# Optimization experiments

Measured on AMD Instinct MI355X. Metric: run time of the kernel, lower is better.

Reference implementation:

```python
import jax, jax.numpy as jnp
import numpy as np

EPS_IN = 1e-5  # torch InstanceNorm1d default eps


def instance_norm(x):
    # x: [B, C, L]; normalize over L per (B, C); no affine (torch default)
    m = jnp.mean(x, axis=-1, keepdims=True)
    v = jnp.var(x, axis=-1, keepdims=True)
    return (x - m) / jnp.sqrt(v + EPS_IN)


def conv1x1(x, w, b):
    # x: [B, Cin, L], w: [Cout, Cin], b: [Cout]
    return jnp.einsum('bcl,oc->bol', x, w) + b[None, :, None]


def _window_indices(L_dec, L_enc, window, stride):
    # static (numpy) window layout matching the torch while-loop
    starts = list(range(0, L_dec, stride))
    dec_ends = [min(s + window, L_dec) for s in starts]
    enc_se = [(int(s * L_enc / L_dec), min(int(e * L_enc / L_dec), L_enc))
              for s, e in zip(starts, dec_ends)]
    max_enc = max(ee - es for es, ee in enc_se)
    ar_d = np.arange(window)
    ar_e = np.arange(max_enc)
    dec_idx = np.stack([np.clip(s + ar_d, 0, L_dec - 1) for s in starts])          # [NW, Wd]
    dec_valid = np.stack([(s + ar_d) < e for s, e in zip(starts, dec_ends)])       # [NW, Wd]
    enc_idx = np.stack([np.clip(es + ar_e, 0, L_enc - 1) for es, ee in enc_se])    # [NW, We]
    enc_valid = np.stack([(es + ar_e) < ee for es, ee in enc_se])                  # [NW, We]
    return (jnp.asarray(dec_idx), jnp.asarray(dec_valid),
            jnp.asarray(enc_idx), jnp.asarray(enc_valid))


def setup_inputs() -> dict:
    key = jax.random.key(0)
    ks = jax.random.split(key, 16)
    B, Cd, Ce, Ld, Le = 4, 512, 256, 4096, 8192
    H = 4 * Cd  # mlp hidden
    s = 0.02
    return {
        'x_decoder': jax.random.normal(ks[0], (B, Cd, Ld), jnp.float32),
        'x_encoder': jax.random.normal(ks[1], (B, Ce, Le), jnp.float32),
        'wq': jax.random.normal(ks[2], (Cd, Cd), jnp.float32) * s,
        'bq': jnp.zeros((Cd,), jnp.float32),
        'wk': jax.random.normal(ks[3], (Cd, Ce), jnp.float32) * s,
        'bk': jnp.zeros((Cd,), jnp.float32),
        'wv': jax.random.normal(ks[4], (Cd, Ce), jnp.float32) * s,
        'bv': jnp.zeros((Cd,), jnp.float32),
        'wo': jax.random.normal(ks[5], (Cd, Cd), jnp.float32) * s,
        'bo': jnp.zeros((Cd,), jnp.float32),
        'w1': jax.random.normal(ks[6], (H, Cd), jnp.float32) * s,
        'b1': jnp.zeros((H,), jnp.float32),
        'w2': jax.random.normal(ks[7], (Cd, H), jnp.float32) * s,
        'b2': jnp.zeros((Cd,), jnp.float32),
    }


NUM_HEADS = 8
WINDOW = 256
STRIDE = 192  # int(256 * (1 - 0.25))


def reference(x_decoder, x_encoder, wq, bq, wk, bk, wv, bv, wo, bo, w1, b1, w2, b2):
    B, Cd, Ld = x_decoder.shape
    Le = x_encoder.shape[-1]
    nh, hd = NUM_HEADS, Cd // NUM_HEADS
    residual = x_decoder

    q = instance_norm(conv1x1(x_decoder, wq, bq))
    k = instance_norm(conv1x1(x_encoder, wk, bk))
    v = instance_norm(conv1x1(x_encoder, wv, bv))

    # [B, C, L] -> [B, nh, L, hd]
    q = q.reshape(B, nh, hd, Ld).transpose(0, 1, 3, 2)
    k = k.reshape(B, nh, hd, Le).transpose(0, 1, 3, 2)
    v = v.reshape(B, nh, hd, Le).transpose(0, 1, 3, 2)

    dec_idx, dec_valid, enc_idx, enc_valid = _window_indices(Ld, Le, WINDOW, STRIDE)
    # gather all windows at once
    qw = q[:, :, dec_idx, :]  # [B, nh, NW, Wd, hd]
    kw = k[:, :, enc_idx, :]  # [B, nh, NW, We, hd]
    vw = v[:, :, enc_idx, :]

    scale = hd ** -0.5
    scores = jnp.einsum('bhnqd,bhnkd->bhnqk', qw, kw) * scale
    scores = jnp.where(enc_valid[None, None, :, None, :], scores, jnp.float32(-1e30))
    attn = jax.nn.softmax(scores, axis=-1)
    win = jnp.einsum('bhnqk,bhnkd->bhnqd', attn, vw)
    win = win * dec_valid[None, None, :, :, None].astype(win.dtype)

    # scatter-add overlapping windows then average by overlap count
    flat_idx = dec_idx.reshape(-1)  # [NW*Wd]
    out = jnp.zeros((B, nh, Ld, hd), win.dtype).at[:, :, flat_idx, :].add(
        win.reshape(B, nh, -1, hd))
    counts = jnp.zeros((Ld,), win.dtype).at[flat_idx].add(
        dec_valid.reshape(-1).astype(win.dtype))
    out = out / jnp.clip(counts, 1e-8)[None, None, :, None]

    attn_out = out.transpose(0, 1, 3, 2).reshape(B, Cd, Ld)
    x = instance_norm(conv1x1(attn_out, wo, bo)) + residual

    # AttentionMLP1D (dropout inactive in eval)
    h = jax.nn.gelu(conv1x1(x, w1, b1), approximate=False)
    y = instance_norm(conv1x1(h, w2, b2))
    return y + x
```

## Files before the change

kernel.cpp:

```cpp
#include <hip/hip_runtime.h>
#include <hip/hip_bf16.h>
#include <math.h>
#include <stdint.h>

#define LDD 4096
#define LEE 8192
#define CDIM 512
#define CENC 256
#define HDIM 2048
#define NB 4
#define NHEAD 8
#define HD 64
#define NWIN 22
#define WINQ 256
#define WSTRIDE 192
#define KVS 1024

typedef __attribute__((ext_vector_type(8))) short bf16x8;
typedef __attribute__((ext_vector_type(8))) unsigned short u16x8;
typedef __attribute__((ext_vector_type(4))) float f32x4;
typedef __attribute__((ext_vector_type(16))) float f32x16;
typedef __attribute__((ext_vector_type(2))) unsigned int u32x2;
typedef __attribute__((ext_vector_type(4))) unsigned int u32x4;
typedef unsigned short ushort_t;

__device__ __forceinline__ uint32_t pack2(float lo, float hi) {
    return ((__float_as_uint(hi) + 0x8000u) & 0xffff0000u) |
           ((__float_as_uint(lo) + 0x8000u) >> 16);
}
__device__ __forceinline__ ushort_t bfc(float x) {
    return (ushort_t)((__float_as_uint(x) + 0x8000u) >> 16);
}
__device__ __forceinline__ float bf2f(ushort_t u) {
    return __uint_as_float(((uint32_t)u) << 16);
}
__device__ __forceinline__ void gload16(const void* g, void* l) {
    __builtin_amdgcn_global_load_lds(
        (const __attribute__((address_space(1))) void*)g,
        (__attribute__((address_space(3))) void*)l, 16, 0, 0);
}
__device__ __forceinline__ float gelu_fast(float x) {
    float z = fabsf(x) * 0.70710678f;
    float t = 1.0f / fmaf(0.3275911f, z, 1.0f);
    float p = t * fmaf(t, fmaf(t, fmaf(t, fmaf(t, 1.061405429f, -1.453152027f),
                                        1.421413741f), -0.284496736f), 0.254829592f);
    float e = __expf(-z * z);
    float erfz = fmaf(-p, e, 1.0f);
    float sgn = copysignf(erfz, x);
    return 0.5f * x * (1.0f + sgn);
}

struct Cvt6Args {
    const float* src[6];
    ushort_t* dst[6];
    int n[6];
};
__global__ __launch_bounds__(256)
void cvt6(Cvt6Args a)
{
    int seg = blockIdx.y;
    int i = (blockIdx.x * 256 + threadIdx.x) * 4;
    if (i < a.n[seg]) {
        float4 v = *reinterpret_cast<const float4*>(&a.src[seg][i]);
        u32x2 p; p[0] = pack2(v.x, v.y); p[1] = pack2(v.z, v.w);
        *reinterpret_cast<u32x2*>(&a.dst[seg][i]) = p;
    }
}

__global__ __launch_bounds__(256)
void bias_stack(const float* __restrict__ bk, const float* __restrict__ bv,
                float* __restrict__ bkv)
{
    int t = blockIdx.x * 256 + threadIdx.x;
    bkv[t] = (t < 512) ? bk[t] : bv[t - 512];
}

__global__ __launch_bounds__(256)
void tcvt(const float* __restrict__ in, ushort_t* __restrict__ outb, int C, int L)
{
    __shared__ float T[64][65];
    int l0 = blockIdx.x * 64, c0 = blockIdx.y * 64, b = blockIdx.z;
    int tid = threadIdx.x;
    int ll = tid & 63, cq = tid >> 6;
    #pragma unroll
    for (int i = 0; i < 16; ++i) {
        int c = cq + i * 4;
        T[c][ll] = in[((size_t)b * C + c0 + c) * L + l0 + ll];
    }
    __syncthreads();
    int cc = tid & 63, lq = tid >> 6;
    #pragma unroll
    for (int i = 0; i < 16; ++i) {
        int l = lq + i * 4;
        outb[((size_t)b * L + l0 + l) * C + c0 + cc] = bfc(T[cc][l]);
    }
}

template<int EPI, int STATS>
__global__ __launch_bounds__(256)
void mgemm2(const ushort_t* __restrict__ A, const ushort_t* __restrict__ Wt,
            const float* __restrict__ bias, ushort_t* __restrict__ Out,
            float* __restrict__ part, int M, int N, int K)
{
    __shared__ __align__(16) ushort_t As[2][8192];
    __shared__ __align__(16) ushort_t Bs[2][8192];

    int Nt = gridDim.x;
    int flat = blockIdx.y * Nt + blockIdx.x;
    int nwg = Nt * gridDim.y;
    int swz = (flat & 7) * (nwg >> 3) + (flat >> 3);
    int nb = swz % Nt, mb = swz / Nt;
    int b = blockIdx.z;
    int m0 = mb * 128, n0 = nb * 128;

    int tid = threadIdx.x;
    int lane = tid & 63;
    int w = tid >> 6;
    int q16 = lane & 15, g = lane >> 4;
    int wr = w >> 1, wc = w & 1;

    const ushort_t* Ag[4]; const ushort_t* Wg[4];
    #pragma unroll
    for (int i = 0; i < 4; ++i) {
        int gran = w * 256 + i * 64 + lane;
        int row = gran >> 3;
        int c8 = (gran & 7) ^ (row & 7);
        Ag[i] = A + ((size_t)b * M + m0 + row) * K + c8 * 8;
        Wg[i] = Wt + ((size_t)(n0 + row)) * K + c8 * 8;
    }

    f32x4 acc[4][4];
    #pragma unroll
    for (int mt = 0; mt < 4; ++mt)
        #pragma unroll
        for (int nt = 0; nt < 4; ++nt) {
            acc[mt][nt][0] = 0.f; acc[mt][nt][1] = 0.f;
            acc[mt][nt][2] = 0.f; acc[mt][nt][3] = 0.f;
        }

    #pragma unroll
    for (int i = 0; i < 4; ++i) {
        gload16(Ag[i], &As[0][w * 2048 + i * 512]);
        gload16(Wg[i], &Bs[0][w * 2048 + i * 512]);
    }

    int NTILES = K >> 6;
    for (int kt = 0; kt < NTILES; ++kt) {
        int cur = kt & 1;
        __syncthreads();
        if (kt + 1 < NTILES) {
            int k0 = (kt + 1) << 6;
            #pragma unroll
            for (int i = 0; i < 4; ++i) {
                gload16(Ag[i] + k0, &As[cur ^ 1][w * 2048 + i * 512]);
                gload16(Wg[i] + k0, &Bs[cur ^ 1][w * 2048 + i * 512]);
            }
        }
        const char* Ab = (const char*)&As[cur][0];
        const char* Bb = (const char*)&Bs[cur][0];
        bf16x8 ka[4][2], kb[4][2];
        #pragma unroll
        for (int mt = 0; mt < 4; ++mt) {
            int r = wr * 64 + mt * 16 + q16;
            int rb = r * 128;
            int sw8 = (r & 7) << 4;
            ka[mt][0] = *reinterpret_cast<const bf16x8*>(Ab + rb + ((g * 16) ^ sw8));
            ka[mt][1] = *reinterpret_cast<const bf16x8*>(Ab + rb + ((64 + g * 16) ^ sw8));
        }
        #pragma unroll
        for (int nt = 0; nt < 4; ++nt) {
            int r = wc * 64 + nt * 16 + q16;
            int rb = r * 128;
            int sw8 = (r & 7) << 4;
            kb[nt][0] = *reinterpret_cast<const bf16x8*>(Bb + rb + ((g * 16) ^ sw8));
            kb[nt][1] = *reinterpret_cast<const bf16x8*>(Bb + rb + ((64 + g * 16) ^ sw8));
        }
        #pragma unroll
        for (int mt = 0; mt < 4; ++mt)
            #pragma unroll
            for (int nt = 0; nt < 4; ++nt) {
                acc[mt][nt] = __builtin_amdgcn_mfma_f32_16x16x32_bf16(kb[nt][0], ka[mt][0], acc[mt][nt], 0, 0, 0);
                acc[mt][nt] = __builtin_amdgcn_mfma_f32_16x16x32_bf16(kb[nt][1], ka[mt][1], acc[mt][nt], 0, 0, 0);
            }
    }

    float4 bv4[4];
    #pragma unroll
    for (int nt = 0; nt < 4; ++nt)
        bv4[nt] = *reinterpret_cast<const float4*>(&bias[n0 + wc * 64 + nt * 16 + g * 4]);

    float s_[4][4], q_[4][4];
    if (STATS) {
        #pragma unroll
        for (int nt = 0; nt < 4; ++nt)
            #pragma unroll
            for (int r = 0; r < 4; ++r) { s_[nt][r] = 0.f; q_[nt][r] = 0.f; }
    }

    #pragma unroll
    for (int mt = 0; mt < 4; ++mt) {
        int m = m0 + wr * 64 + mt * 16 + q16;
        size_t rowoff = ((size_t)b * M + m) * N;
        #pragma unroll
        for (int nt = 0; nt < 4; ++nt) {
            float vv[4];
            #pragma unroll
            for (int r = 0; r < 4; ++r) {
                float val = acc[mt][nt][r] + ((const float*)&bv4[nt])[r];
                if (EPI == 1) val = gelu_fast(val);
                if (STATS) { s_[nt][r] += val; q_[nt][r] = fmaf(val, val, q_[nt][r]); }
                vv[r] = val;
            }
            u32x2 pk; pk[0] = pack2(vv[0], vv[1]); pk[1] = pack2(vv[2], vv[3]);
            *reinterpret_cast<u32x2*>(&Out[rowoff + n0 + wc * 64 + nt * 16 + g * 4]) = pk;
        }
    }

    if (STATS) {
        __syncthreads();
        float* SS = (float*)&As[0][0];
        float* SQ = (float*)&Bs[0][0];
        #pragma unroll
        for (int nt = 0; nt < 4; ++nt)
            #pragma unroll
            for (int r = 0; r < 4; ++r) {
                int nl = wc * 64 + nt * 16 + g * 4 + r;
                SS[nl * 33 + wr * 16 + q16] = s_[nt][r];
                SQ[nl * 33 + wr * 16 + q16] = q_[nt][r];
            }
        __syncthreads();
        if (tid < 128) {
            float ts = 0.f, tq = 0.f;
            #pragma unroll 8
            for (int j = 0; j < 32; ++j) { ts += SS[tid * 33 + j]; tq += SQ[tid * 33 + j]; }
            size_t po = (((size_t)b * (M >> 7) + mb) * N + n0 + tid) * 2;
            part[po] = ts; part[po + 1] = tq;
        }
    }
}

__global__ __launch_bounds__(256)
void stats_finish(const float* __restrict__ pq, const float* __restrict__ pkv,
                  float* __restrict__ qm, float* __restrict__ qr,
                  float* __restrict__ vm, float* __restrict__ vr, float qscale)
{
    int id = blockIdx.x * 256 + threadIdx.x;
    int b = id >> 9, c = id & 511;
    float sq = 0.f, qq = 0.f;
    for (int sp = 0; sp < 32; ++sp) {
        size_t po = (((size_t)(b * 32 + sp)) * CDIM + c) * 2;
        sq += pq[po]; qq += pq[po + 1];
    }
    float sk = 0.f, qk = 0.f, sv = 0.f, qv = 0.f;
    for (int sp = 0; sp < 64; ++sp) {
        size_t po = (((size_t)(b * 64 + sp)) * KVS + c) * 2;
        sk += pkv[po]; qk += pkv[po + 1];
        sv += pkv[po + 1024]; qv += pkv[po + 1025];
    }
    float mq = sq / (float)LDD;
    float rq = rsqrtf(qq / (float)LDD - mq * mq + 1e-5f);
    float mk = sk / (float)LEE;
    float rk = rsqrtf(qk / (float)LEE - mk * mk + 1e-5f);
    float mv = sv / (float)LEE;
    qm[id] = mq;
    qr[id] = rq * rk * qscale;
    vm[id] = mv;
    vr[id] = rsqrtf(qv / (float)LEE - mv * mv + 1e-5f);
}

template<int RES>
__global__ __launch_bounds__(256)
void cn_apply_v(const ushort_t* __restrict__ in, const float* __restrict__ part,
                const ushort_t* __restrict__ res, ushort_t* __restrict__ out,
                int L, int SPLITM)
{
    __shared__ float SM[CDIM], SR[CDIM];
    int b = blockIdx.z;
    int tid = threadIdx.x;
    for (int c = tid; c < CDIM; c += 256) {
        float fs = 0.f, fq = 0.f;
        for (int sp = 0; sp < SPLITM; ++sp) {
            size_t po = (((size_t)b * SPLITM + sp) * CDIM + c) * 2;
            fs += part[po]; fq += part[po + 1];
        }
        float mean = fs / (float)L;
        float var = fq / (float)L - mean * mean;
        SM[c] = mean; SR[c] = rsqrtf(var + 1e-5f);
    }
    __syncthreads();
    int c0 = (tid & 63) * 8;
    int l0 = blockIdx.x * 16 + (tid >> 6) * 4;
    float mm[8], rr[8];
    #pragma unroll
    for (int j = 0; j < 8; ++j) { mm[j] = SM[c0 + j]; rr[j] = SR[c0 + j]; }
    #pragma unroll
    for (int i = 0; i < 4; ++i) {
        int l = l0 + i;
        size_t off = ((size_t)b * L + l) * CDIM + c0;
        u16x8 v = *reinterpret_cast<const u16x8*>(in + off);
        u16x8 rv;
        if (RES) rv = *reinterpret_cast<const u16x8*>(res + off);
        u16x8 o;
        #pragma unroll
        for (int j = 0; j < 8; ++j) {
            float y = (bf2f((ushort_t)v[j]) - mm[j]) * rr[j];
            if (RES) y += bf2f((ushort_t)rv[j]);
            o[j] = bfc(y);
        }
        *reinterpret_cast<u16x8*>(out + off) = o;
    }
}

__global__ __launch_bounds__(256)
void cn_apply_t(const ushort_t* __restrict__ in, const float* __restrict__ part,
                const ushort_t* __restrict__ res, float* __restrict__ outf,
                int L, int SPLITM)
{
    __shared__ float SM[64], SR[64];
    __shared__ float T[64][65];
    int b = blockIdx.z;
    int c0 = blockIdx.x * 64;
    int l0 = blockIdx.y * 64;
    int tid = threadIdx.x;
    if (tid < 64) {
        int c = c0 + tid;
        float fs = 0.f, fq = 0.f;
        for (int sp = 0; sp < SPLITM; ++sp) {
            size_t po = (((size_t)b * SPLITM + sp) * CDIM + c) * 2;
            fs += part[po]; fq += part[po + 1];
        }
        float mean = fs / (float)L;
        float var = fq / (float)L - mean * mean;
        SM[tid] = mean; SR[tid] = rsqrtf(var + 1e-5f);
    }
    __syncthreads();
    int cc = tid & 63;
    int lq = tid >> 6;
    float mean = SM[cc], rstd = SR[cc];
    #pragma unroll
    for (int i = 0; i < 16; ++i) {
        int l = l0 + lq + i * 4;
        size_t idx = ((size_t)b * L + l) * CDIM + c0 + cc;
        T[lq + i * 4][cc] = (bf2f(in[idx]) - mean) * rstd + bf2f(res[idx]);
    }
    __syncthreads();
    int ll = tid & 63;
    int cr = tid >> 6;
    #pragma unroll
    for (int i = 0; i < 16; ++i) {
        int c = cr + i * 4;
        outf[((size_t)b * CDIM + c0 + c) * L + l0 + ll] = T[ll][c];
    }
}

__global__ __launch_bounds__(512, 2)
void attn_win_mfma32(const ushort_t* __restrict__ qT, const ushort_t* __restrict__ kvT,
                     const float* __restrict__ qmean, const float* __restrict__ qrs,
                     const float* __restrict__ vmean, const float* __restrict__ vrstd,
                     ushort_t* __restrict__ win)
{
    __shared__ __align__(16) char KB[3][8192];
    __shared__ __align__(16) ushort_t VBv[2][64][68];
    __shared__ float VMS[64], VRS[64], QMS[64], QRS[64];

    int p = blockIdx.x;
    int xcd = p & 7;
    int sub = p >> 3;
    int g9 = xcd * 11 + (sub % 11);
    int hh = sub / 11;
    int n = g9 % 22, b = g9 / 22;

    int s = n * WSTRIDE;
    int es = 2 * s;
    bool tail = (n == NWIN - 1);
    int nch = tail ? 2 : 8;

    int tid = threadIdx.x;
    int lane = tid & 63;
    int w = tid >> 6;
    int l31 = lane & 31;
    int hf = lane >> 5;
    bool active = (!tail) || (w < 2);

    const ushort_t* kbase = kvT + ((size_t)b * LEE + es) * KVS + hh * HD;
    const ushort_t* vbase = kbase + 512;

    int vc8 = tid & 7;
    int vkp = tid >> 3;
    bool vdo = (tid < 256);
    int vcs = (vc8 & 6) << 2;

    int kpos0 = tid >> 3;
    int kc8 = (tid & 7) ^ (kpos0 & 7);
    const ushort_t* ksrc = kbase + (size_t)kpos0 * KVS + kc8 * 8;

    u16x8 qraw[4];
    if (active) {
        int qrow_g = s + w * 32 + l31;
        const ushort_t* qp = qT + ((size_t)b * LDD + qrow_g) * CDIM + hh * HD;
        #pragma unroll
        for (int kd = 0; kd < 4; ++kd)
            qraw[kd] = *reinterpret_cast<const u16x8*>(qp + kd * 16 + hf * 8);
    }
    gload16(ksrc, &KB[0][tid * 16]);
    u16x8 wa0, wb0;
    if (vdo) {
        const ushort_t* src = vbase + (size_t)(2 * vkp) * KVS + vc8 * 8;
        wa0 = *reinterpret_cast<const u16x8*>(src);
        wb0 = *reinterpret_cast<const u16x8*>(src + KVS);
    }
    gload16(ksrc + (size_t)64 * KVS, &KB[1][tid * 16]);
    if (tid < 64) {
        int c = b * CDIM + hh * HD + tid;
        VMS[tid] = vmean[c]; VRS[tid] = vrstd[c];
        QMS[tid] = qmean[c]; QRS[tid] = qrs[c];
    }
    if (vdo) {
        #pragma unroll
        for (int j = 0; j < 8; ++j) {
            int d = vc8 * 8 + j;
            uint32_t dw = (uint32_t)wa0[j] | ((uint32_t)wb0[j] << 16);
            *reinterpret_cast<uint32_t*>(&VBv[0][d][(2 * vkp) ^ vcs]) = dw;
        }
    }
    asm volatile("s_waitcnt lgkmcnt(0)" ::: "memory");
    __builtin_amdgcn_s_barrier();

    bf16x8 bq[4];
    if (active) {
        #pragma unroll
        for (int kd = 0; kd < 4; ++kd) {
            u32x4 pk;
            #pragma unroll
            for (int jj = 0; jj < 4; ++jj) {
                int c0 = kd * 16 + hf * 8 + 2 * jj;
                float y0 = (bf2f((ushort_t)qraw[kd][2 * jj]) - QMS[c0]) * QRS[c0];
                float y1 = (bf2f((ushort_t)qraw[kd][2 * jj + 1]) - QMS[c0 + 1]) * QRS[c0 + 1];
                pk[jj] = pack2(y0, y1);
            }
            bq[kd] = __builtin_bit_cast(bf16x8, pk);
        }
    }

    f32x16 acc0, acc1;
    #pragma unroll
    for (int e = 0; e < 16; ++e) { acc0[e] = 0.f; acc1[e] = 0.f; }
    float ssum = 0.f;
    int swk = (lane & 7) << 4;
    int vrs0 = ((l31 >> 3) & 6) << 2;
    int vrs1 = (((l31 + 32) >> 3) & 6) << 2;

    for (int ch = 0; ch < nch; ++ch) {
        asm volatile("s_waitcnt vmcnt(1) lgkmcnt(0)" ::: "memory");
        __builtin_amdgcn_s_barrier();

        u16x8 wa, wb;
        bool pfv = (ch + 1 < nch);
        if (pfv && vdo) {
            const ushort_t* src = vbase + (size_t)((ch + 1) * 64 + 2 * vkp) * KVS + vc8 * 8;
            wa = *reinterpret_cast<const u16x8*>(src);
            wb = *reinterpret_cast<const u16x8*>(src + KVS);
        }
        if (ch + 2 < nch)
            gload16(ksrc + (size_t)((ch + 2) * 64) * KVS, &KB[(ch + 2) % 3][tid * 16]);

        if (active) {
            f32x16 st0, st1;
            #pragma unroll
            for (int e = 0; e < 16; ++e) { st0[e] = 0.f; st1[e] = 0.f; }
            const char* KA0 = &KB[ch % 3][l31 * 128];
            const char* KA1 = KA0 + 32 * 128;
            __builtin_amdgcn_s_setprio(1);
            #pragma unroll
            for (int kd = 0; kd < 4; ++kd) {
                int co = (kd * 32 + hf * 16) ^ swk;
                bf16x8 ka0 = *reinterpret_cast<const bf16x8*>(KA0 + co);
                bf16x8 ka1 = *reinterpret_cast<const bf16x8*>(KA1 + co);
                st0 = __builtin_amdgcn_mfma_f32_32x32x16_bf16(ka0, bq[kd], st0, 0, 0, 0);
                st1 = __builtin_amdgcn_mfma_f32_32x32x16_bf16(ka1, bq[kd], st1, 0, 0, 0);
            }
            __builtin_amdgcn_s_setprio(0);
            uint32_t pk0[8], pk1[8];
            float ls = 0.f;
            #pragma unroll
            for (int pp = 0; pp < 8; ++pp) {
                float a = exp2f(st0[2 * pp] - 24.f), bb = exp2f(st0[2 * pp + 1] - 24.f);
                float c = exp2f(st1[2 * pp] - 24.f), dd = exp2f(st1[2 * pp + 1] - 24.f);
                ls += (a + bb) + (c + dd);
                pk0[pp] = pack2(a, bb);
                pk1[pp] = pack2(c, dd);
            }
            ssum += ls;
            __builtin_amdgcn_s_setprio(1);
            #pragma unroll
            for (int kc = 0; kc < 4; ++kc) {
                const int sub2 = kc & 1;
                uint32_t pA0, pA1, pA2, pA3;
                if ((kc >> 1) == 0) { pA0 = pk0[4*sub2]; pA1 = pk0[4*sub2+1]; pA2 = pk0[4*sub2+2]; pA3 = pk0[4*sub2+3]; }
                else                { pA0 = pk1[4*sub2]; pA1 = pk1[4*sub2+1]; pA2 = pk1[4*sub2+2]; pA3 = pk1[4*sub2+3]; }
                uint32_t s0 = hf ? pA0 : pA2;
                uint32_t s1 = hf ? pA1 : pA3;
                uint32_t r0 = (uint32_t)__shfl_xor((int)s0, 32);
                uint32_t r1 = (uint32_t)__shfl_xor((int)s1, 32);
                u32x4 bt;
                bt[0] = hf ? r0 : pA0;
                bt[1] = hf ? r1 : pA1;
                bt[2] = hf ? pA2 : r0;
                bt[3] = hf ? pA3 : r1;
                bf16x8 pbf = __builtin_bit_cast(bf16x8, bt);
                int ko = kc * 16 + hf * 8;
                const uint32_t* vr0p = reinterpret_cast<const uint32_t*>(&VBv[ch & 1][l31][ko ^ vrs0]);
                const uint32_t* vr1p = reinterpret_cast<const uint32_t*>(&VBv[ch & 1][l31 + 32][ko ^ vrs1]);
                u32x2 alo = *reinterpret_cast<const u32x2*>(vr0p);
                u32x2 ahi = *reinterpret_cast<const u32x2*>(vr0p + 2);
                u32x2 blo = *reinterpret_cast<const u32x2*>(vr1p);
                u32x2 bhi = *reinterpret_cast<const u32x2*>(vr1p + 2);
                u32x4 va0u, va1u;
                va0u[0] = alo[0]; va0u[1] = alo[1]; va0u[2] = ahi[0]; va0u[3] = ahi[1];
                va1u[0] = blo[0]; va1u[1] = blo[1]; va1u[2] = bhi[0]; va1u[3] = bhi[1];
                bf16x8 va0 = __builtin_bit_cast(bf16x8, va0u);
                bf16x8 va1 = __builtin_bit_cast(bf16x8, va1u);
                acc0 = __builtin_amdgcn_mfma_f32_32x32x16_bf16(va0, pbf, acc0, 0, 0, 0);
                acc1 = __builtin_amdgcn_mfma_f32_32x32x16_bf16(va1, pbf, acc1, 0, 0, 0);
            }
            __builtin_amdgcn_s_setprio(0);
        }

        if (pfv && vdo) {
            #pragma unroll
            for (int j = 0; j < 8; ++j) {
                int d = vc8 * 8 + j;
                uint32_t dw = (uint32_t)wa[j] | ((uint32_t)wb[j] << 16);
                *reinterpret_cast<uint32_t*>(&VBv[(ch + 1) & 1][d][(2 * vkp) ^ vcs]) = dw;
            }
        }
    }

    if (active) {
        float stot = ssum + __shfl_xor(ssum, 32);
        float rs = 1.f / stot;
        size_t wbase = (((size_t)(b * NHEAD + hh) * NWIN + n) * WINQ + (size_t)(w * 32 + l31)) * HD;
        #pragma unroll
        for (int p4 = 0; p4 < 4; ++p4) {
            int d0 = p4 * 8 + hf * 4;
            float o0[4], o1[4];
            #pragma unroll
            for (int e = 0; e < 4; ++e) {
                o0[e] = VRS[d0 + e] * (acc0[4 * p4 + e] * rs - VMS[d0 + e]);
                o1[e] = VRS[32 + d0 + e] * (acc1[4 * p4 + e] * rs - VMS[32 + d0 + e]);
            }
            u32x2 w0, w1v;
            w0[0] = pack2(o0[0], o0[1]); w0[1] = pack2(o0[2], o0[3]);
            w1v[0] = pack2(o1[0], o1[1]); w1v[1] = pack2(o1[2], o1[3]);
            *reinterpret_cast<u32x2*>(&win[wbase + p4 * 8 + hf * 4]) = w0;
            *reinterpret_cast<u32x2*>(&win[wbase + 32 + p4 * 8 + hf * 4]) = w1v;
        }
    }
}

__global__ __launch_bounds__(256)
void attn_finalize(const ushort_t* __restrict__ win, ushort_t* __restrict__ outT)
{
    int l0 = blockIdx.x * 64;
    int hh = blockIdx.y, b = blockIdx.z;
    int tid = threadIdx.x;
    int d2 = tid & 31;
    int lq = tid >> 5;
    #pragma unroll
    for (int i = 0; i < 8; ++i) {
        int ll = lq + i * 8;
        int l = l0 + ll;
        int n1 = min(NWIN - 1, l / WSTRIDE);
        int n0 = (l >= 64) ? ((l - 64) / WSTRIDE) : 0;
        float a0 = 0.f, a1 = 0.f;
        for (int nn = n0; nn <= n1; ++nn) {
            int qrow = l - nn * WSTRIDE;
            uint32_t v = *reinterpret_cast<const uint32_t*>(
                &win[(((size_t)(b * NHEAD + hh) * NWIN + nn) * WINQ + qrow) * HD + d2 * 2]);
            a0 += bf2f((ushort_t)(v & 0xffffu));
            a1 += bf2f((ushort_t)(v >> 16));
        }
        float inv = 1.f / (float)(n1 - n0 + 1);
        uint32_t o = pack2(a0 * inv, a1 * inv);
        *reinterpret_cast<uint32_t*>(
            &outT[((size_t)b * LDD + l) * CDIM + hh * HD + d2 * 2]) = o;
    }
}

extern "C" void kernel_launch(void* const* d_in, const int* in_sizes, int n_in,
                              void* d_out, int out_size, void* d_ws, size_t ws_size,
                              hipStream_t stream)
{
    const float* x_dec = (const float*)d_in[0];
    const float* x_enc = (const float*)d_in[1];
    const float* wq = (const float*)d_in[2];
    const float* bq = (const float*)d_in[3];
    const float* wk = (const float*)d_in[4];
    const float* bk = (const float*)d_in[5];
    const float* wv = (const float*)d_in[6];
    const float* bv = (const float*)d_in[7];
    const float* wo = (const float*)d_in[8];
    const float* bo = (const float*)d_in[9];
    const float* w1 = (const float*)d_in[10];
    const float* b1 = (const float*)d_in[11];
    const float* w2 = (const float*)d_in[12];
    const float* b2 = (const float*)d_in[13];
    float* out = (float*)d_out;

    char* base = (char*)d_ws;
    ushort_t* wqb  = (ushort_t*)(base);
    ushort_t* wkvb = (ushort_t*)(base + 524288);
    ushort_t* wob  = (ushort_t*)(base + 1048576);
    ushort_t* w1b  = (ushort_t*)(base + 1572864);
    ushort_t* w2b  = (ushort_t*)(base + 3670016);
    ushort_t* x_decT_b = (ushort_t*)(base + 5767168);
    ushort_t* q_pre    = (ushort_t*)(base + 22544384);
    ushort_t* kvT      = (ushort_t*)(base + 39321600);
    ushort_t* x_encT_b = (ushort_t*)(base + 106430464);
    ushort_t* winb     = (ushort_t*)(base + 123207680);
    float*    partQ    = (float*)(base + 169345024);
    float*    partKV   = (float*)(base + 170393600);
    float*    qm       = (float*)(base + 172490752);
    float*    qr       = qm + 2048;
    float*    vm       = qr + 2048;
    float*    vrs      = vm + 2048;
    float*    bkv      = vrs + 2048;
    ushort_t* attn_outT = x_encT_b;
    ushort_t* xo_pre   = q_pre;
    ushort_t* hT       = kvT;
    ushort_t* y_pre    = winb;

    dim3 blk(256);
    dim3 blk512(512);

    Cvt6Args ca;
    ca.src[0] = wq; ca.src[1] = wk; ca.src[2] = wv;
    ca.src[3] = wo; ca.src[4] = w1; ca.src[5] = w2;
    ca.dst[0] = wqb; ca.dst[1] = wkvb; ca.dst[2] = wkvb + 131072;
    ca.dst[3] = wob; ca.dst[4] = w1b; ca.dst[5] = w2b;
    ca.n[0] = 262144; ca.n[1] = 131072; ca.n[2] = 131072;
    ca.n[3] = 262144; ca.n[4] = 1048576; ca.n[5] = 1048576;
    cvt6<<<dim3(1024, 6), blk, 0, stream>>>(ca);
    bias_stack<<<dim3(4), blk, 0, stream>>>(bk, bv, bkv);

    tcvt<<<dim3(LDD / 64, CDIM / 64, NB), blk, 0, stream>>>(x_dec, x_decT_b, CDIM, LDD);
    tcvt<<<dim3(LEE / 64, CENC / 64, NB), blk, 0, stream>>>(x_enc, x_encT_b, CENC, LEE);

    const float QSCALE = 0.125f * 1.4426950408889634f;

    mgemm2<0,1><<<dim3(CDIM / 128, LDD / 128, NB), blk, 0, stream>>>(x_decT_b, wqb, bq, q_pre, partQ, LDD, CDIM, CDIM);
    mgemm2<0,1><<<dim3(KVS / 128, LEE / 128, NB), blk, 0, stream>>>(x_encT_b, wkvb, bkv, kvT, partKV, LEE, KVS, CENC);
    stats_finish<<<dim3(8), blk, 0, stream>>>(partQ, partKV, qm, qr, vm, vrs, QSCALE);

    attn_win_mfma32<<<dim3(NWIN * NHEAD * NB), blk512, 0, stream>>>(q_pre, kvT, qm, qr, vm, vrs, winb);
    attn_finalize<<<dim3(LDD / 64, NHEAD, NB), blk, 0, stream>>>(winb, attn_outT);

    mgemm2<0,1><<<dim3(CDIM / 128, LDD / 128, NB), blk, 0, stream>>>(attn_outT, wob, bo, xo_pre, partQ, LDD, CDIM, CDIM);
    cn_apply_v<1><<<dim3(LDD / 16, 1, NB), blk, 0, stream>>>(xo_pre, partQ, x_decT_b, xo_pre, LDD, LDD / 128);

    mgemm2<1,0><<<dim3(HDIM / 128, LDD / 128, NB), blk, 0, stream>>>(xo_pre, w1b, b1, hT, nullptr, LDD, HDIM, CDIM);

    mgemm2<0,1><<<dim3(CDIM / 128, LDD / 128, NB), blk, 0, stream>>>(hT, w2b, b2, y_pre, partQ, LDD, CDIM, HDIM);
    cn_apply_t<<<dim3(CDIM / 64, LDD / 64, NB), blk, 0, stream>>>(y_pre, partQ, xo_pre, out, LDD, LDD / 128);

    (void)in_sizes; (void)n_in; (void)out_size; (void)ws_size;
}
```

Before: 331.8 us.

## Replace 128x128 GEMM with 256x256 eight-wave ping-pong pipelined kernel

Replaces the 128x128, 4-wave double-buffered bf16 MFMA GEMM with a 256x256 tile, 8-wave kernel. It splits each K-step into quarter tiles, staged through four LDS slots with explicit vmcnt/lgkmcnt waits, barriers and s_setprio around the MFMA bursts. The aim is more data reuse per LDS load and better overlap of global loads with matrix math. Statistic partials and stats_finish are re-parameterised for the new row-block count. The risk is that the larger tiles cut the grid to 128 blocks for the N=512 GEMMs, which may leave many CUs idle.

```diff
diff --git a/kernel.cpp b/kernel.cpp
--- a/kernel.cpp
+++ b/kernel.cpp
@@ -97,13 +97,13 @@
 }
 
 template<int EPI, int STATS>
-__global__ __launch_bounds__(256)
-void mgemm2(const ushort_t* __restrict__ A, const ushort_t* __restrict__ Wt,
-            const float* __restrict__ bias, ushort_t* __restrict__ Out,
-            float* __restrict__ part, int M, int N, int K)
-{
-    __shared__ __align__(16) ushort_t As[2][8192];
-    __shared__ __align__(16) ushort_t Bs[2][8192];
+__global__ __launch_bounds__(512, 1)
+void mgemm8p(const ushort_t* __restrict__ A, const ushort_t* __restrict__ Wt,
+             const float* __restrict__ bias, ushort_t* __restrict__ Out,
+             float* __restrict__ part, int M, int N, int K)
+{
+    __shared__ __align__(16) ushort_t Asl[4][8192];
+    __shared__ __align__(16) ushort_t Bsl[4][8192];
 
     int Nt = gridDim.x;
     int flat = blockIdx.y * Nt + blockIdx.x;
@@ -111,83 +111,205 @@
     int swz = (flat & 7) * (nwg >> 3) + (flat >> 3);
     int nb = swz % Nt, mb = swz / Nt;
     int b = blockIdx.z;
-    int m0 = mb * 128, n0 = nb * 128;
+    int m0 = mb * 256, n0 = nb * 256;
 
     int tid = threadIdx.x;
     int lane = tid & 63;
     int w = tid >> 6;
-    int q16 = lane & 15, g = lane >> 4;
-    int wr = w >> 1, wc = w & 1;
-
-    const ushort_t* Ag[4]; const ushort_t* Wg[4];
-    #pragma unroll
-    for (int i = 0; i < 4; ++i) {
-        int gran = w * 256 + i * 64 + lane;
-        int row = gran >> 3;
-        int c8 = (gran & 7) ^ (row & 7);
-        Ag[i] = A + ((size_t)b * M + m0 + row) * K + c8 * 8;
-        Wg[i] = Wt + ((size_t)(n0 + row)) * K + c8 * 8;
-    }
-
-    f32x4 acc[4][4];
-    #pragma unroll
-    for (int mt = 0; mt < 4; ++mt)
+    int q16 = lane & 15, g4 = lane >> 4;
+    int wr = w >> 2, wc = w & 3;
+
+    const ushort_t* Ap[2][2]; const ushort_t* Bp[2][2];
+    #pragma unroll
+    for (int j = 0; j < 2; ++j) {
+        int g = w * 128 + j * 64 + lane;
+        int row = g >> 3;
+        int c8 = (g & 7) ^ (row & 7);
+        #pragma unroll
+        for (int hh = 0; hh < 2; ++hh) {
+            Ap[hh][j] = A + ((size_t)b * M + m0 + hh * 128 + row) * K + c8 * 8;
+            Bp[hh][j] = Wt + ((size_t)(n0 + hh * 128 + row)) * K + c8 * 8;
+        }
+    }
+    int dbase = w * 2048;
+
+    auto stageA = [&](int slot, int hh, int k0) {
+        char* d = (char*)&Asl[0][0] + slot * 16384 + dbase;
+        gload16(Ap[hh][0] + k0, d);
+        gload16(Ap[hh][1] + k0, d + 1024);
+    };
+    auto stageB = [&](int slot, int hh, int k0) {
+        char* d = (char*)&Bsl[0][0] + slot * 16384 + dbase;
+        gload16(Bp[hh][0] + k0, d);
+        gload16(Bp[hh][1] + k0, d + 1024);
+    };
+
+    f32x4 acc[8][4];
+    #pragma unroll
+    for (int mt = 0; mt < 8; ++mt)
         #pragma unroll
         for (int nt = 0; nt < 4; ++nt) {
             acc[mt][nt][0] = 0.f; acc[mt][nt][1] = 0.f;
             acc[mt][nt][2] = 0.f; acc[mt][nt][3] = 0.f;
         }
 
-    #pragma unroll
-    for (int i = 0; i < 4; ++i) {
-        gload16(Ag[i], &As[0][w * 2048 + i * 512]);
-        gload16(Wg[i], &Bs[0][w * 2048 + i * 512]);
-    }
-
-    int NTILES = K >> 6;
-    for (int kt = 0; kt < NTILES; ++kt) {
-        int cur = kt & 1;
-        __syncthreads();
-        if (kt + 1 < NTILES) {
-            int k0 = (kt + 1) << 6;
-            #pragma unroll
-            for (int i = 0; i < 4; ++i) {
-                gload16(Ag[i] + k0, &As[cur ^ 1][w * 2048 + i * 512]);
-                gload16(Wg[i] + k0, &Bs[cur ^ 1][w * 2048 + i * 512]);
-            }
-        }
-        const char* Ab = (const char*)&As[cur][0];
-        const char* Bb = (const char*)&Bs[cur][0];
+    const char* As0 = (const char*)&Asl[wr][0];
+    const char* As1 = (const char*)&Asl[2 + wr][0];
+    const char* Bs0 = (const char*)&Bsl[wc >> 1][0];
+    const char* Bs1 = (const char*)&Bsl[2 + (wc >> 1)][0];
+
+    auto ldka = [&](const char* sp, int rbase, bf16x8 (&ka)[4][2]) {
+        #pragma unroll
+        for (int mt = 0; mt < 4; ++mt) {
+            int r = rbase + mt * 16 + q16;
+            int rb = r * 128, sw8 = (r & 7) << 4;
+            ka[mt][0] = *reinterpret_cast<const bf16x8*>(sp + rb + ((g4 * 16) ^ sw8));
+            ka[mt][1] = *reinterpret_cast<const bf16x8*>(sp + rb + ((64 + g4 * 16) ^ sw8));
+        }
+    };
+    auto ldkb = [&](const char* sp, bf16x8 (&kb)[4][2]) {
+        #pragma unroll
+        for (int nt = 0; nt < 4; ++nt) {
+            int r = (wc & 1) * 64 + nt * 16 + q16;
+            int rb = r * 128, sw8 = (r & 7) << 4;
+            kb[nt][0] = *reinterpret_cast<const bf16x8*>(sp + rb + ((g4 * 16) ^ sw8));
+            kb[nt][1] = *reinterpret_cast<const bf16x8*>(sp + rb + ((64 + g4 * 16) ^ sw8));
+        }
+    };
+
+    int NT = K >> 6;
+    int NI = NT >> 1;
+
+    stageB(0, 0, 0);
+    stageB(1, 1, 0);
+    stageA(0, 0, 0);
+    stageA(1, 1, 0);
+    stageB(2, 0, 64);
+    stageB(3, 1, 64);
+    stageA(2, 0, 64);
+
+    for (int i = 0; i < NI; ++i) {
         bf16x8 ka[4][2], kb[4][2];
-        #pragma unroll
-        for (int mt = 0; mt < 4; ++mt) {
-            int r = wr * 64 + mt * 16 + q16;
-            int rb = r * 128;
-            int sw8 = (r & 7) << 4;
-            ka[mt][0] = *reinterpret_cast<const bf16x8*>(Ab + rb + ((g * 16) ^ sw8));
-            ka[mt][1] = *reinterpret_cast<const bf16x8*>(Ab + rb + ((64 + g * 16) ^ sw8));
-        }
-        #pragma unroll
-        for (int nt = 0; nt < 4; ++nt) {
-            int r = wc * 64 + nt * 16 + q16;
-            int rb = r * 128;
-            int sw8 = (r & 7) << 4;
-            kb[nt][0] = *reinterpret_cast<const bf16x8*>(Bb + rb + ((g * 16) ^ sw8));
-            kb[nt][1] = *reinterpret_cast<const bf16x8*>(Bb + rb + ((64 + g * 16) ^ sw8));
-        }
+        int kB1 = (2 * i + 1) * 64;
+        int kA  = (2 * i + 2) * 64;
+        int kC  = (2 * i + 3) * 64;
+        bool pf = (i + 1 < NI);
+
+        asm volatile("s_waitcnt vmcnt(6) lgkmcnt(0)" ::: "memory");
+        __builtin_amdgcn_s_barrier();
+        asm volatile("" ::: "memory");
+        stageA(3, 1, kB1);
+        ldka(As0, 0, ka); ldkb(Bs0, kb);
+        __builtin_amdgcn_s_setprio(1);
         #pragma unroll
         for (int mt = 0; mt < 4; ++mt)
             #pragma unroll
-            for (int nt = 0; nt < 4; ++nt) {
+            for (int nt = 0; nt < 2; ++nt) {
                 acc[mt][nt] = __builtin_amdgcn_mfma_f32_16x16x32_bf16(kb[nt][0], ka[mt][0], acc[mt][nt], 0, 0, 0);
                 acc[mt][nt] = __builtin_amdgcn_mfma_f32_16x16x32_bf16(kb[nt][1], ka[mt][1], acc[mt][nt], 0, 0, 0);
             }
+        __builtin_amdgcn_s_setprio(0);
+        asm volatile("s_waitcnt lgkmcnt(0)" ::: "memory");
+        __builtin_amdgcn_s_barrier();
+        asm volatile("" ::: "memory");
+        if (pf) stageB(0, 0, kA);
+        __builtin_amdgcn_s_setprio(1);
+        #pragma unroll
+        for (int mt = 0; mt < 4; ++mt)
+            #pragma unroll
+            for (int nt = 2; nt < 4; ++nt) {
+                acc[mt][nt] = __builtin_amdgcn_mfma_f32_16x16x32_bf16(kb[nt][0], ka[mt][0], acc[mt][nt], 0, 0, 0);
+                acc[mt][nt] = __builtin_amdgcn_mfma_f32_16x16x32_bf16(kb[nt][1], ka[mt][1], acc[mt][nt], 0, 0, 0);
+            }
+        __builtin_amdgcn_s_setprio(0);
+        asm volatile("s_waitcnt lgkmcnt(0)" ::: "memory");
+        __builtin_amdgcn_s_barrier();
+        asm volatile("" ::: "memory");
+        if (pf) stageB(1, 1, kA);
+        ldka(As0, 64, ka);
+        __builtin_amdgcn_s_setprio(1);
+        #pragma unroll
+        for (int mt = 0; mt < 4; ++mt)
+            #pragma unroll
+            for (int nt = 0; nt < 2; ++nt) {
+                acc[4 + mt][nt] = __builtin_amdgcn_mfma_f32_16x16x32_bf16(kb[nt][0], ka[mt][0], acc[4 + mt][nt], 0, 0, 0);
+                acc[4 + mt][nt] = __builtin_amdgcn_mfma_f32_16x16x32_bf16(kb[nt][1], ka[mt][1], acc[4 + mt][nt], 0, 0, 0);
+            }
+        __builtin_amdgcn_s_setprio(0);
+        asm volatile("s_waitcnt lgkmcnt(0)" ::: "memory");
+        __builtin_amdgcn_s_barrier();
+        asm volatile("" ::: "memory");
+        if (pf) stageA(0, 0, kA);
+        __builtin_amdgcn_s_setprio(1);
+        #pragma unroll
+        for (int mt = 0; mt < 4; ++mt)
+            #pragma unroll
+            for (int nt = 2; nt < 4; ++nt) {
+                acc[4 + mt][nt] = __builtin_amdgcn_mfma_f32_16x16x32_bf16(kb[nt][0], ka[mt][0], acc[4 + mt][nt], 0, 0, 0);
+                acc[4 + mt][nt] = __builtin_amdgcn_mfma_f32_16x16x32_bf16(kb[nt][1], ka[mt][1], acc[4 + mt][nt], 0, 0, 0);
+            }
+        __builtin_amdgcn_s_setprio(0);
+        if (pf) asm volatile("s_waitcnt vmcnt(6) lgkmcnt(0)" ::: "memory");
+        else    asm volatile("s_waitcnt vmcnt(0) lgkmcnt(0)" ::: "memory");
+        __builtin_amdgcn_s_barrier();
+        asm volatile("" ::: "memory");
+        if (pf) stageA(1, 1, kA);
+        ldka(As1, 0, ka); ldkb(Bs1, kb);
+        __builtin_amdgcn_s_setprio(1);
+        #pragma unroll
+        for (int mt = 0; mt < 4; ++mt)
+            #pragma unroll
+            for (int nt = 0; nt < 2; ++nt) {
+                acc[mt][nt] = __builtin_amdgcn_mfma_f32_16x16x32_bf16(kb[nt][0], ka[mt][0], acc[mt][nt], 0, 0, 0);
+                acc[mt][nt] = __builtin_amdgcn_mfma_f32_16x16x32_bf16(kb[nt][1], ka[mt][1], acc[mt][nt], 0, 0, 0);
+            }
+        __builtin_amdgcn_s_setprio(0);
+        asm volatile("s_waitcnt lgkmcnt(0)" ::: "memory");
+        __builtin_amdgcn_s_barrier();
+        asm volatile("" ::: "memory");
+        if (pf) stageB(2, 0, kC);
+        __builtin_amdgcn_s_setprio(1);
+        #pragma unroll
+        for (int mt = 0; mt < 4; ++mt)
+            #pragma unroll
+            for (int nt = 2; nt < 4; ++nt) {
+                acc[mt][nt] = __builtin_amdgcn_mfma_f32_16x16x32_bf16(kb[nt][0], ka[mt][0], acc[mt][nt], 0, 0, 0);
+                acc[mt][nt] = __builtin_amdgcn_mfma_f32_16x16x32_bf16(kb[nt][1], ka[mt][1], acc[mt][nt], 0, 0, 0);
+            }
+        __builtin_amdgcn_s_setprio(0);
+        asm volatile("s_waitcnt lgkmcnt(0)" ::: "memory");
+        __builtin_amdgcn_s_barrier();
+        asm volatile("" ::: "memory");
+        if (pf) stageB(3, 1, kC);
+        ldka(As1, 64, ka);
+        __builtin_amdgcn_s_setprio(1);
+        #pragma unroll
+        for (int mt = 0; mt < 4; ++mt)
+            #pragma unroll
+            for (int nt = 0; nt < 2; ++nt) {
+                acc[4 + mt][nt] = __builtin_amdgcn_mfma_f32_16x16x32_bf16(kb[nt][0], ka[mt][0], acc[4 + mt][nt], 0, 0, 0);
+                acc[4 + mt][nt] = __builtin_amdgcn_mfma_f32_16x16x32_bf16(kb[nt][1], ka[mt][1], acc[4 + mt][nt], 0, 0, 0);
+            }
+        __builtin_amdgcn_s_setprio(0);
+        asm volatile("s_waitcnt lgkmcnt(0)" ::: "memory");
+        __builtin_amdgcn_s_barrier();
+        asm volatile("" ::: "memory");
+        if (pf) stageA(2, 0, kC);
+        __builtin_amdgcn_s_setprio(1);
+        #pragma unroll
+        for (int mt = 0; mt < 4; ++mt)
+            #pragma unroll
+            for (int nt = 2; nt < 4; ++nt) {
+                acc[4 + mt][nt] = __builtin_amdgcn_mfma_f32_16x16x32_bf16(kb[nt][0], ka[mt][0], acc[4 + mt][nt], 0, 0, 0);
+                acc[4 + mt][nt] = __builtin_amdgcn_mfma_f32_16x16x32_bf16(kb[nt][1], ka[mt][1], acc[4 + mt][nt], 0, 0, 0);
+            }
+        __builtin_amdgcn_s_setprio(0);
     }
 
     float4 bv4[4];
     #pragma unroll
     for (int nt = 0; nt < 4; ++nt)
-        bv4[nt] = *reinterpret_cast<const float4*>(&bias[n0 + wc * 64 + nt * 16 + g * 4]);
+        bv4[nt] = *reinterpret_cast<const float4*>(&bias[n0 + wc * 64 + nt * 16 + g4 * 4]);
 
     float s_[4][4], q_[4][4];
     if (STATS) {
@@ -198,8 +320,8 @@
     }
 
     #pragma unroll
-    for (int mt = 0; mt < 4; ++mt) {
-        int m = m0 + wr * 64 + mt * 16 + q16;
+    for (int mt = 0; mt < 8; ++mt) {
+        int m = m0 + wr * 128 + mt * 16 + q16;
         size_t rowoff = ((size_t)b * M + m) * N;
         #pragma unroll
         for (int nt = 0; nt < 4; ++nt) {
@@ -212,28 +334,28 @@
                 vv[r] = val;
             }
             u32x2 pk; pk[0] = pack2(vv[0], vv[1]); pk[1] = pack2(vv[2], vv[3]);
-            *reinterpret_cast<u32x2*>(&Out[rowoff + n0 + wc * 64 + nt * 16 + g * 4]) = pk;
+            *reinterpret_cast<u32x2*>(&Out[rowoff + n0 + wc * 64 + nt * 16 + g4 * 4]) = pk;
         }
     }
 
     if (STATS) {
         __syncthreads();
-        float* SS = (float*)&As[0][0];
-        float* SQ = (float*)&Bs[0][0];
+        float* SS = (float*)&Asl[0][0];
+        float* SQ = (float*)&Bsl[0][0];
         #pragma unroll
         for (int nt = 0; nt < 4; ++nt)
             #pragma unroll
             for (int r = 0; r < 4; ++r) {
-                int nl = wc * 64 + nt * 16 + g * 4 + r;
+                int nl = wc * 64 + nt * 16 + g4 * 4 + r;
                 SS[nl * 33 + wr * 16 + q16] = s_[nt][r];
                 SQ[nl * 33 + wr * 16 + q16] = q_[nt][r];
             }
         __syncthreads();
-        if (tid < 128) {
+        if (tid < 256) {
             float ts = 0.f, tq = 0.f;
             #pragma unroll 8
             for (int j = 0; j < 32; ++j) { ts += SS[tid * 33 + j]; tq += SQ[tid * 33 + j]; }
-            size_t po = (((size_t)b * (M >> 7) + mb) * N + n0 + tid) * 2;
+            size_t po = (((size_t)b * (M >> 8) + mb) * N + n0 + tid) * 2;
             part[po] = ts; part[po + 1] = tq;
         }
     }
@@ -242,18 +364,19 @@
 __global__ __launch_bounds__(256)
 void stats_finish(const float* __restrict__ pq, const float* __restrict__ pkv,
                   float* __restrict__ qm, float* __restrict__ qr,
-                  float* __restrict__ vm, float* __restrict__ vr, float qscale)
+                  float* __restrict__ vm, float* __restrict__ vr,
+                  float qscale, int SQ_, int SKV_)
 {
     int id = blockIdx.x * 256 + threadIdx.x;
     int b = id >> 9, c = id & 511;
     float sq = 0.f, qq = 0.f;
-    for (int sp = 0; sp < 32; ++sp) {
-        size_t po = (((size_t)(b * 32 + sp)) * CDIM + c) * 2;
+    for (int sp = 0; sp < SQ_; ++sp) {
+        size_t po = (((size_t)(b * SQ_ + sp)) * CDIM + c) * 2;
         sq += pq[po]; qq += pq[po + 1];
     }
     float sk = 0.f, qk = 0.f, sv = 0.f, qv = 0.f;
-    for (int sp = 0; sp < 64; ++sp) {
-        size_t po = (((size_t)(b * 64 + sp)) * KVS + c) * 2;
+    for (int sp = 0; sp < SKV_; ++sp) {
+        size_t po = (((size_t)(b * SKV_ + sp)) * KVS + c) * 2;
         sk += pkv[po]; qk += pkv[po + 1];
         sv += pkv[po + 1024]; qv += pkv[po + 1025];
     }
@@ -648,20 +771,20 @@
 
     const float QSCALE = 0.125f * 1.4426950408889634f;
 
-    mgemm2<0,1><<<dim3(CDIM / 128, LDD / 128, NB), blk, 0, stream>>>(x_decT_b, wqb, bq, q_pre, partQ, LDD, CDIM, CDIM);
-    mgemm2<0,1><<<dim3(KVS / 128, LEE / 128, NB), blk, 0, stream>>>(x_encT_b, wkvb, bkv, kvT, partKV, LEE, KVS, CENC);
-    stats_finish<<<dim3(8), blk, 0, stream>>>(partQ, partKV, qm, qr, vm, vrs, QSCALE);
+    mgemm8p<0,1><<<dim3(CDIM / 256, LDD / 256, NB), blk512, 0, stream>>>(x_decT_b, wqb, bq, q_pre, partQ, LDD, CDIM, CDIM);
+    mgemm8p<0,1><<<dim3(KVS / 256, LEE / 256, NB), blk512, 0, stream>>>(x_encT_b, wkvb, bkv, kvT, partKV, LEE, KVS, CENC);
+    stats_finish<<<dim3(8), blk, 0, stream>>>(partQ, partKV, qm, qr, vm, vrs, QSCALE, LDD / 256, LEE / 256);
 
     attn_win_mfma32<<<dim3(NWIN * NHEAD * NB), blk512, 0, stream>>>(q_pre, kvT, qm, qr, vm, vrs, winb);
     attn_finalize<<<dim3(LDD / 64, NHEAD, NB), blk, 0, stream>>>(winb, attn_outT);
 
-    mgemm2<0,1><<<dim3(CDIM / 128, LDD / 128, NB), blk, 0, stream>>>(attn_outT, wob, bo, xo_pre, partQ, LDD, CDIM, CDIM);
-    cn_apply_v<1><<<dim3(LDD / 16, 1, NB), blk, 0, stream>>>(xo_pre, partQ, x_decT_b, xo_pre, LDD, LDD / 128);
-
-    mgemm2<1,0><<<dim3(HDIM / 128, LDD / 128, NB), blk, 0, stream>>>(xo_pre, w1b, b1, hT, nullptr, LDD, HDIM, CDIM);
-
-    mgemm2<0,1><<<dim3(CDIM / 128, LDD / 128, NB), blk, 0, stream>>>(hT, w2b, b2, y_pre, partQ, LDD, CDIM, HDIM);
-    cn_apply_t<<<dim3(CDIM / 64, LDD / 64, NB), blk, 0, stream>>>(y_pre, partQ, xo_pre, out, LDD, LDD / 128);
+    mgemm8p<0,1><<<dim3(CDIM / 256, LDD / 256, NB), blk512, 0, stream>>>(attn_outT, wob, bo, xo_pre, partQ, LDD, CDIM, CDIM);
+    cn_apply_v<1><<<dim3(LDD / 16, 1, NB), blk, 0, stream>>>(xo_pre, partQ, x_decT_b, xo_pre, LDD, LDD / 256);
+
+    mgemm8p<1,0><<<dim3(HDIM / 256, LDD / 256, NB), blk512, 0, stream>>>(xo_pre, w1b, b1, hT, nullptr, LDD, HDIM, CDIM);
+
+    mgemm8p<0,1><<<dim3(CDIM / 256, LDD / 256, NB), blk512, 0, stream>>>(hT, w2b, b2, y_pre, partQ, LDD, CDIM, HDIM);
+    cn_apply_t<<<dim3(CDIM / 64, LDD / 64, NB), blk, 0, stream>>>(y_pre, partQ, xo_pre, out, LDD, LDD / 256);
 
     (void)in_sizes; (void)n_in; (void)out_size; (void)ws_size;
 }
```

Result: slower. 362.4 us (+9.2%).
